# Performance work log

Hardware: AMD Instinct MI355X
Metric: run time of the kernel (lower is better)

The kernel has to match this reference:

```python
import jax, jax.numpy as jnp
import numpy as np

H = 32        # query heads
KV = 8        # kv heads
HD = 128      # head_dim
EPS = 1e-6
THETA = 1e6
T = 2048
D = 4096


def _rms_norm(x, w):
    # x: [T, heads, HD]
    var = jnp.mean(jnp.square(x), axis=-1, keepdims=True)
    return x * jax.lax.rsqrt(var + EPS) * w


def _rope(x, cos, sin):
    # NEOX-style rotary: split last dim in halves. x: [T, heads, HD]
    x1, x2 = jnp.split(x, 2, axis=-1)
    return jnp.concatenate([x1 * cos - x2 * sin, x2 * cos + x1 * sin], axis=-1)


def setup_inputs() -> dict:
    key = jax.random.key(0)
    k1, k2, k3 = jax.random.split(key, 3)
    s = 1.0 / np.sqrt(D)
    return {
        "positions": jnp.arange(T, dtype=jnp.int32),
        "hidden_states": jax.random.normal(k1, (T, D), dtype=jnp.float32),
        "w_qkv": jax.random.normal(k2, (D, (H + 2 * KV) * HD), dtype=jnp.float32) * s,
        "q_norm_w": jnp.ones((HD,), dtype=jnp.float32),
        "k_norm_w": jnp.ones((HD,), dtype=jnp.float32),
        "w_o": jax.random.normal(k3, (H * HD, D), dtype=jnp.float32) * s,
    }


def reference(positions, hidden_states, w_qkv, q_norm_w, k_norm_w, w_o):
    scale = HD ** -0.5
    qkv = hidden_states @ w_qkv                              # [T, (H+2KV)*HD]
    q = qkv[:, : H * HD].reshape(T, H, HD)
    k = qkv[:, H * HD : (H + KV) * HD].reshape(T, KV, HD)
    v = qkv[:, (H + KV) * HD :].reshape(T, KV, HD)

    # per-head RMSNorm on q/k (Qwen3 QK-norm)
    q = _rms_norm(q, q_norm_w)
    k = _rms_norm(k, k_norm_w)

    # RoPE
    inv_freq = 1.0 / (THETA ** (jnp.arange(0, HD, 2, dtype=jnp.float32) / HD))
    freqs = positions.astype(jnp.float32)[:, None] * inv_freq  # [T, HD/2]
    cos = jnp.cos(freqs)[:, None, :]                            # [T, 1, HD/2]
    sin = jnp.sin(freqs)[:, None, :]
    q = _rope(q, cos, sin)
    k = _rope(k, cos, sin)

    # GQA: repeat kv heads
    rep = H // KV
    k = jnp.repeat(k, rep, axis=1)                           # [T, H, HD]
    v = jnp.repeat(v, rep, axis=1)

    # causal SDPA
    scores = jnp.einsum("thd,shd->hts", q, k) * scale        # [H, T, T]
    causal = jnp.tril(jnp.ones((T, T), dtype=bool))
    scores = jnp.where(causal[None], scores, jnp.finfo(scores.dtype).min)
    probs = jax.nn.softmax(scores, axis=-1)
    attn = jnp.einsum("hts,shd->thd", probs, v).reshape(T, H * HD)

    return attn @ w_o                                        # [T, D]
```

## Files before the change

### kernel.cpp

```cpp
#include <hip/hip_runtime.h>

#define TT   2048
#define DD   4096
#define NH   32
#define NKVH 8
#define HDM  128
#define KD   4096
#define NQKV 6144

typedef unsigned short u16;
typedef short v8s __attribute__((ext_vector_type(8)));
typedef float v4f __attribute__((ext_vector_type(4)));

#define QSCALE 0.12751744547734565f
#define EOFF   17.312340490667562f

__device__ __forceinline__ u16 f2bf(float f) {
    unsigned u = __builtin_bit_cast(unsigned, f);
    u += 0x7fffu + ((u >> 16) & 1u);
    return (u16)(u >> 16);
}
__device__ __forceinline__ float bf2f(u16 h) {
    return __builtin_bit_cast(float, ((unsigned)h) << 16);
}
__device__ __forceinline__ void gl2lds16(const void* g, void* l) {
    using gv = const __attribute__((address_space(1))) void;
    using lv = __attribute__((address_space(3))) void;
    __builtin_amdgcn_global_load_lds((gv*)g, (lv*)l, 16, 0, 0);
}

__device__ __forceinline__ void transpose_tile64(const float* __restrict__ in,
                                                 u16* __restrict__ out,
                                                 int K, int N, int n0, int k0,
                                                 float* tile, int t) {
    int rc = t >> 4, cc = (t & 15) * 4;
#pragma unroll
    for (int p = 0; p < 4; ++p) {
        int k = p * 16 + rc;
        float4 v = *(const float4*)&in[(size_t)(k0 + k) * N + n0 + cc];
        tile[k * 65 + cc] = v.x; tile[k * 65 + cc + 1] = v.y;
        tile[k * 65 + cc + 2] = v.z; tile[k * 65 + cc + 3] = v.w;
    }
    __syncthreads();
    int rn = t >> 3, ck = (t & 7) * 8;
#pragma unroll
    for (int p = 0; p < 2; ++p) {
        int n = p * 32 + rn;
        v8s tv;
#pragma unroll
        for (int j = 0; j < 8; ++j) tv[j] = (short)f2bf(tile[(ck + j) * 65 + n]);
        *(v8s*)&out[(size_t)(n0 + n) * K + k0 + ck] = tv;
    }
}

__global__ __launch_bounds__(256) void prep_all_kernel(const float* __restrict__ hidden,
                                                       u16* __restrict__ hid_bf,
                                                       const int* __restrict__ positions,
                                                       float* __restrict__ cosT,
                                                       float* __restrict__ sinT,
                                                       const float* __restrict__ w_qkv,
                                                       u16* __restrict__ wqkv_t) {
    __shared__ float tile[64 * 65];
    int b = blockIdx.x;
    if (b < 4096) {
        size_t i = ((size_t)b * 256 + threadIdx.x) * 8;
        float4 a = *(const float4*)&hidden[i];
        float4 c = *(const float4*)&hidden[i + 4];
        v8s tv;
        tv[0] = (short)f2bf(a.x); tv[1] = (short)f2bf(a.y);
        tv[2] = (short)f2bf(a.z); tv[3] = (short)f2bf(a.w);
        tv[4] = (short)f2bf(c.x); tv[5] = (short)f2bf(c.y);
        tv[6] = (short)f2bf(c.z); tv[7] = (short)f2bf(c.w);
        *(v8s*)&hid_bf[i] = tv;
    } else if (b < 4608) {
        int idx = (b - 4096) * 256 + threadIdx.x;
        int tp = idx >> 6, i = idx & 63;
        float invf = exp2f(-(float)i * 0.31143075889569023f);
        float f = (float)positions[tp] * invf;
        cosT[idx] = cosf(f);
        sinT[idx] = sinf(f);
    } else {
        int bx = b - 4608;
        int n0 = (bx % 96) * 64, k0 = (bx / 96) * 64;
        transpose_tile64(w_qkv, wqkv_t, 4096, NQKV, n0, k0, tile, threadIdx.x);
    }
}

__global__ __launch_bounds__(256) void gemm_bt_kernel(
    const u16* __restrict__ A, const u16* __restrict__ Bt, float* __restrict__ C, int N)
{
    __shared__ __align__(16) u16 smem[16896];
    u16* As = smem;
    u16* Bs = smem + 8192;
    int tid = threadIdx.x;
    int wave = tid >> 6, lane = tid & 63;
    int quad = lane >> 4, l15 = lane & 15;
    int lm = l15 & 7;
    int wm = wave >> 1, wn = wave & 1;
    int m0 = blockIdx.y * 128, n0 = blockIdx.x * 128;

    v4f acc[4][4];
    v4f z4 = {0.f, 0.f, 0.f, 0.f};
#pragma unroll
    for (int mi = 0; mi < 4; ++mi)
#pragma unroll
        for (int ni = 0; ni < 4; ++ni) acc[mi][ni] = z4;

    int rsub = lane >> 3;
    int cg = (lane & 7) ^ rsub;
    const u16* Ag = &A[(size_t)m0 * KD + cg * 8];
    const u16* Bg = &Bt[(size_t)n0 * KD + cg * 8];

    for (int k0 = 0; k0 < KD; k0 += 64) {
        __syncthreads();
#pragma unroll
        for (int c = 0; c < 4; ++c) {
            int ch = wave * 4 + c;
            int row = ch * 8 + rsub;
            gl2lds16(&Ag[(size_t)row * KD + k0], &As[ch * 512]);
            gl2lds16(&Bg[(size_t)row * KD + k0], &Bs[ch * 512]);
        }
        __syncthreads();
#pragma unroll
        for (int ks = 0; ks < 2; ++ks) {
            v8s af[4], bfr[4];
#pragma unroll
            for (int mi = 0; mi < 4; ++mi) {
                int ar = wm * 64 + mi * 16 + l15;
                af[mi] = *(const v8s*)&As[ar * 64 + ((((ks << 2) + quad) ^ lm) << 3)];
            }
#pragma unroll
            for (int ni = 0; ni < 4; ++ni) {
                int br = wn * 64 + ni * 16 + l15;
                bfr[ni] = *(const v8s*)&Bs[br * 64 + ((((ks << 2) + quad) ^ lm) << 3)];
            }
#pragma unroll
            for (int mi = 0; mi < 4; ++mi)
#pragma unroll
                for (int ni = 0; ni < 4; ++ni)
                    acc[mi][ni] = __builtin_amdgcn_mfma_f32_16x16x32_bf16(
                        af[mi], bfr[ni], acc[mi][ni], 0, 0, 0);
        }
    }
#pragma unroll
    for (int mi = 0; mi < 4; ++mi)
#pragma unroll
        for (int ni = 0; ni < 4; ++ni)
#pragma unroll
            for (int r = 0; r < 4; ++r)
                C[(size_t)(m0 + wm * 64 + mi * 16 + quad * 4 + r) * N +
                  (n0 + wn * 64 + ni * 16 + l15)] = acc[mi][ni][r];
}

__global__ __launch_bounds__(512, 2) void gemm_qkv384_kernel(
    const u16* __restrict__ A, const u16* __restrict__ Bt,
    const float* __restrict__ qw, const float* __restrict__ kw,
    const float* __restrict__ cosT, const float* __restrict__ sinT,
    u16* __restrict__ Qb, u16* __restrict__ Kb, u16* __restrict__ Vt)
{
    __shared__ __align__(16) char smem_raw[131072];
    u16* lds = (u16*)smem_raw;
    const int tid = threadIdx.x;
    const int wave = tid >> 6, lane = tid & 63;
    const int quad = lane >> 4, l15 = lane & 15, lm = l15 & 7;
    const int wm = wave >> 2, wn = wave & 3;
    const int m0 = blockIdx.y * 128, n0 = blockIdx.x * 384;

    v4f acc[2][4][3];
    v4f z4 = {0.f, 0.f, 0.f, 0.f};
#pragma unroll
    for (int nh = 0; nh < 2; ++nh)
#pragma unroll
        for (int mi = 0; mi < 4; ++mi)
#pragma unroll
            for (int ni = 0; ni < 3; ++ni) acc[nh][mi][ni] = z4;

    const int rsub = lane >> 3;
    const int cg = (lane & 7) ^ rsub;
    const int ch0 = wave * 2;
    const int g0 = (quad ^ lm) << 3;
    const int g1 = ((4 + quad) ^ lm) << 3;

    const u16* AgR0 = &A[((size_t)m0 + (ch0 + 0) * 8 + rsub) * KD + cg * 8];
    const u16* AgR1 = &A[((size_t)m0 + (ch0 + 1) * 8 + rsub) * KD + cg * 8];
    const u16* BgR0 = &Bt[((size_t)n0 + (ch0 + 0) * 8 + rsub) * KD + cg * 8];
    const u16* BgR1 = &Bt[((size_t)n0 + (ch0 + 1) * 8 + rsub) * KD + cg * 8];

#define STAGE_AH(tt) do { \
    int _b = ((tt) & 1) * 32768; \
    gl2lds16(AgR0 + (size_t)(tt) * 64, &lds[_b + (ch0 + 0) * 512]); \
    gl2lds16(AgR1 + (size_t)(tt) * 64, &lds[_b + (ch0 + 1) * 512]); \
  } while (0)
#define STAGE_BH(tt, h) do { \
    int _b = ((tt) & 1) * 32768 + 8192; \
    gl2lds16(BgR0 + (size_t)(h) * 128 * KD + (size_t)(tt) * 64, \
             &lds[_b + (h) * 8192 + (ch0 + 0) * 512]); \
    gl2lds16(BgR1 + (size_t)(h) * 128 * KD + (size_t)(tt) * 64, \
             &lds[_b + (h) * 8192 + (ch0 + 1) * 512]); \
  } while (0)

    v8s af[4], bfr[3];

#define PHASEX(BO, G, NHI, RDA, STAGE_CODE, WAIT_CODE) do { \
    if (RDA) { \
      _Pragma("unroll") \
      for (int mi = 0; mi < 4; ++mi) \
        af[mi] = *(const v8s*)&lds[(BO) + (wm * 64 + mi * 16 + l15) * 64 + (G)]; \
    } \
    _Pragma("unroll") \
    for (int ni = 0; ni < 3; ++ni) \
      bfr[ni] = *(const v8s*)&lds[(BO) + 8192 + \
                   (wn * 96 + (NHI) * 48 + ni * 16 + l15) * 64 + (G)]; \
    STAGE_CODE; \
    __builtin_amdgcn_s_barrier(); \
    asm volatile("s_waitcnt lgkmcnt(0)" ::: "memory"); \
    __builtin_amdgcn_s_setprio(1); \
    _Pragma("unroll") \
    for (int mi = 0; mi < 4; ++mi) \
      _Pragma("unroll") \
      for (int ni = 0; ni < 3; ++ni) \
        acc[NHI][mi][ni] = __builtin_amdgcn_mfma_f32_16x16x32_bf16( \
            af[mi], bfr[ni], acc[NHI][mi][ni], 0, 0, 0); \
    __builtin_amdgcn_s_setprio(0); \
    WAIT_CODE; \
    __builtin_amdgcn_s_barrier(); \
  } while (0)

#define VM0 asm volatile("s_waitcnt vmcnt(0)" ::: "memory")

#define TILE_MAIN(BO, TT1) do { \
    PHASEX(BO, g0, 0, 1, { STAGE_AH(TT1); STAGE_BH(TT1, 0); }, {}); \
    PHASEX(BO, g0, 1, 0, { STAGE_BH(TT1, 1); }, {}); \
    PHASEX(BO, g1, 0, 1, { STAGE_BH(TT1, 2); }, {}); \
    PHASEX(BO, g1, 1, 0, {}, { VM0; }); \
  } while (0)

    STAGE_AH(0); STAGE_BH(0, 0); STAGE_BH(0, 1); STAGE_BH(0, 2);
    VM0;
    __builtin_amdgcn_s_barrier();

#pragma unroll 2
    for (int t = 0; t < 62; ++t) {
        const int bo = (t & 1) * 32768;
        TILE_MAIN(bo, t + 1);
    }
    TILE_MAIN(0, 63);
    PHASEX(32768, g0, 0, 1, {}, {});
    PHASEX(32768, g0, 1, 0, {}, {});
    PHASEX(32768, g1, 0, 1, {}, {});
    PHASEX(32768, g1, 1, 0, {}, {});
#undef TILE_MAIN
#undef PHASEX
#undef STAGE_AH
#undef STAGE_BH
#undef VM0

    u16* Ct = lds;
    const int t0q = blockIdx.y * 128;
    __syncthreads();
#pragma unroll
    for (int nh = 0; nh < 2; ++nh)
#pragma unroll
        for (int mi = 0; mi < 4; ++mi)
#pragma unroll
            for (int ni = 0; ni < 3; ++ni)
#pragma unroll
                for (int r = 0; r < 4; ++r)
                    Ct[(wm * 64 + mi * 16 + quad * 4 + r) * 392 +
                       wn * 96 + nh * 48 + ni * 16 + l15] = f2bf(acc[nh][mi][ni][r]);
    __syncthreads();
    if (tid < 384) {
        const int row = tid & 127, hh = tid >> 7;
        const int head = blockIdx.x * 3 + hh;
        if (head < 40) {
            const float* w = (head < 32) ? qw : kw;
            float ss = 0.f;
            for (int i = 0; i < 128; ++i) {
                float x = bf2f(Ct[row * 392 + hh * 128 + i]);
                ss += x * x;
            }
            float rs = rsqrtf(ss * (1.0f / 128.0f) + 1e-6f);
            if (head < 32) rs *= QSCALE;
            const int ti = t0q + row;
            for (int i = 0; i < 64; ++i) {
                float x1 = bf2f(Ct[row * 392 + hh * 128 + i]) * rs * w[i];
                float x2 = bf2f(Ct[row * 392 + hh * 128 + 64 + i]) * rs * w[64 + i];
                float c = cosT[ti * 64 + i], s = sinT[ti * 64 + i];
                Ct[row * 392 + hh * 128 + i]      = f2bf(x1 * c - x2 * s);
                Ct[row * 392 + hh * 128 + 64 + i] = f2bf(x2 * c + x1 * s);
            }
        }
    }
    __syncthreads();
#pragma unroll
    for (int hh = 0; hh < 3; ++hh) {
        const int head = blockIdx.x * 3 + hh;
        if (head < 40) {
            u16* dst = (head < 32) ? &Qb[((size_t)head * TT + t0q) * HDM]
                                   : &Kb[((size_t)(head - 32) * TT + t0q) * HDM];
            for (int cix = tid; cix < 128 * 16; cix += 512) {
                int row = cix >> 4, part = (cix & 15) * 8;
                v8s tv;
#pragma unroll
                for (int j = 0; j < 8; ++j) tv[j] = (short)Ct[row * 392 + hh * 128 + part + j];
                *(v8s*)&dst[row * HDM + part] = tv;
            }
        } else {
            const int kvh = head - 40;
            for (int cix = tid; cix < 128 * 16; cix += 512) {
                int hd = cix >> 4, tb = cix & 15;
                v8s tv;
#pragma unroll
                for (int j = 0; j < 8; ++j) tv[j] = (short)Ct[(tb * 8 + j) * 392 + hh * 128 + hd];
                *(v8s*)&Vt[((size_t)kvh * HDM + hd) * TT + t0q + tb * 8] = tv;
            }
        }
    }
}

__global__ __launch_bounds__(256) void attn_plus_kernel(
    const u16* __restrict__ Qb, const u16* __restrict__ Kb,
    const u16* __restrict__ Vt, u16* __restrict__ Ob,
    const float* __restrict__ w_o, u16* __restrict__ wo_t)
{
    __shared__ __align__(16) char smem_raw[40960];
    int tid = threadIdx.x;
    if (blockIdx.x >= 1024) {
        int bx = blockIdx.x - 1024;
        int n0 = (bx & 63) * 64, k0 = (bx >> 6) * 64;
        transpose_tile64(w_o, wo_t, 4096, 4096, n0, k0, (float*)smem_raw, tid);
        return;
    }
    u16* Kl = (u16*)smem_raw;
    u16* Vl = (u16*)(smem_raw + 16384);
    u16* Pl = (u16*)(smem_raw + 32768);
    int wave = tid >> 6, lane = tid & 63;
    int quad = lane >> 4, l15 = lane & 15;
    int idx = blockIdx.x;
    int h = idx & 31;
    int qb = 31 - (idx >> 5);
    int kv = h >> 2;
    int q0 = qb * 64;
    int lm = l15 & 7;

    v8s qf[4];
    {
        const u16* qr = &Qb[((size_t)h * TT + q0 + wave * 16 + l15) * HDM];
#pragma unroll
        for (int ks = 0; ks < 4; ++ks) qf[ks] = *(const v8s*)&qr[ks * 32 + quad * 8];
    }

    v4f z4 = {0.f, 0.f, 0.f, 0.f};
    v4f of[8];
#pragma unroll
    for (int i = 0; i < 8; ++i) of[i] = z4;
    float lsum[4];
#pragma unroll
    for (int r = 0; r < 4; ++r) lsum[r] = 0.f;
    u16* Pw = &Pl[wave * 1024];

    for (int s0 = 0; s0 <= q0; s0 += 64) {
        __syncthreads();
#pragma unroll
        for (int c = 0; c < 4; ++c) {
            int ch = wave * 4 + c;
            int rk = ch * 4 + (lane >> 4);
            int ck = (lane & 15) ^ (rk & 7);
            gl2lds16(&Kb[((size_t)kv * TT + s0 + rk) * HDM + ck * 8], &Kl[ch * 512]);
            int rv = ch * 8 + (lane >> 3);
            int cv = (lane & 7) ^ (rv & 7);
            gl2lds16(&Vt[((size_t)kv * HDM + rv) * TT + s0 + cv * 8], &Vl[ch * 512]);
        }
        __syncthreads();
        v4f sf[4];
#pragma unroll
        for (int nt = 0; nt < 4; ++nt) {
            v4f cacc = z4;
#pragma unroll
            for (int ks = 0; ks < 4; ++ks)
                cacc = __builtin_amdgcn_mfma_f32_16x16x32_bf16(
                    qf[ks],
                    *(const v8s*)&Kl[(nt * 16 + l15) * 128 + (((ks * 4 + quad) ^ lm) << 3)],
                    cacc, 0, 0, 0);
            sf[nt] = cacc;
        }
        if (s0 == q0) {
#pragma unroll
            for (int nt = 0; nt < 4; ++nt) {
                int sg = s0 + nt * 16 + l15;
#pragma unroll
                for (int r = 0; r < 4; ++r) {
                    int qg = q0 + wave * 16 + quad * 4 + r;
                    if (sg > qg) sf[nt][r] = -3.0e38f;
                }
            }
        }
#pragma unroll
        for (int nt = 0; nt < 4; ++nt)
#pragma unroll
            for (int r = 0; r < 4; ++r) {
                float p = exp2f(sf[nt][r] - EOFF);
                sf[nt][r] = p;
                lsum[r] += p;
            }
#pragma unroll
        for (int nt = 0; nt < 4; ++nt)
#pragma unroll
            for (int r = 0; r < 4; ++r) {
                int row = quad * 4 + r;
                int pch = ((nt << 1) + (l15 >> 3)) ^ (row & 7);
                Pw[row * 64 + pch * 8 + (l15 & 7)] = f2bf(sf[nt][r]);
            }
#pragma unroll
        for (int sub = 0; sub < 2; ++sub) {
            v8s pa = *(const v8s*)&Pw[l15 * 64 + ((((sub << 2) + quad) ^ lm) << 3)];
#pragma unroll
            for (int nt = 0; nt < 8; ++nt)
                of[nt] = __builtin_amdgcn_mfma_f32_16x16x32_bf16(
                    pa,
                    *(const v8s*)&Vl[(nt * 16 + l15) * 64 + ((((sub << 2) + quad) ^ lm) << 3)],
                    of[nt], 0, 0, 0);
        }
    }
#pragma unroll
    for (int off = 1; off < 16; off <<= 1)
#pragma unroll
        for (int r = 0; r < 4; ++r) lsum[r] += __shfl_xor(lsum[r], off, 64);
    float invl[4];
#pragma unroll
    for (int r = 0; r < 4; ++r) invl[r] = 1.0f / lsum[r];
#pragma unroll
    for (int nt = 0; nt < 8; ++nt)
#pragma unroll
        for (int r = 0; r < 4; ++r)
            Ob[(size_t)(q0 + wave * 16 + quad * 4 + r) * (NH * HDM) + h * HDM + nt * 16 + l15] =
                f2bf(of[nt][r] * invl[r]);
}

extern "C" void kernel_launch(void* const* d_in, const int* in_sizes, int n_in,
                              void* d_out, int out_size, void* d_ws, size_t ws_size,
                              hipStream_t stream)
{
    (void)in_sizes; (void)n_in; (void)out_size; (void)ws_size;
    const int*   positions = (const int*)d_in[0];
    const float* hidden    = (const float*)d_in[1];
    const float* w_qkv     = (const float*)d_in[2];
    const float* q_norm_w  = (const float*)d_in[3];
    const float* k_norm_w  = (const float*)d_in[4];
    const float* w_o       = (const float*)d_in[5];
    float* out = (float*)d_out;
    char* ws = (char*)d_ws;
    char* ob = (char*)d_out;

    u16* hid_bf = (u16*)(ws + 0);
    u16* attnO  = (u16*)(ws + 0);
    u16* wqkv_t = (u16*)(ws + (size_t)16777216);
    u16* wo_t   = (u16*)(ws + (size_t)16777216);

    u16*   Qb   = (u16*)(ob + 0);
    u16*   Kb   = (u16*)(ob + (size_t)16777216);
    u16*   Vt   = (u16*)(ob + (size_t)20971520);
    float* cosT = (float*)(ob + (size_t)25165824);
    float* sinT = (float*)(ob + (size_t)25690112);

    prep_all_kernel<<<10752, 256, 0, stream>>>(hidden, hid_bf, positions, cosT, sinT,
                                               w_qkv, wqkv_t);

    gemm_qkv384_kernel<<<dim3(16, 16), 512, 0, stream>>>(
        hid_bf, wqkv_t, q_norm_w, k_norm_w, cosT, sinT, Qb, Kb, Vt);

    attn_plus_kernel<<<5120, 256, 0, stream>>>(Qb, Kb, Vt, attnO, w_o, wo_t);

    gemm_bt_kernel<<<dim3(32, 16), 256, 0, stream>>>(attnO, wo_t, out, 4096);
}
```

Before: 456.9 us.

## Pipeline output GEMM with double-buffered LDS and 128x256 tiles

Replaces the simple single-buffered output projection GEMM with a 512-thread, 128x256-tile kernel. It double-buffers global-to-LDS loads so the next K tile is fetched while MFMAs run, and raises wave priority around the MFMAs. The QKV kernel also drops an explicit lgkmcnt wait, changes its LDS row stride from 392 to 390 to reduce bank conflicts, and reorders V-transpose indexing. The tradeoffs are higher LDS and register pressure, and dropping the lgkmcnt wait depends on compiler-inserted waits for correctness.

```diff
diff --git a/kernel.cpp b/kernel.cpp
--- a/kernel.cpp
+++ b/kernel.cpp
@@ -14,6 +14,7 @@
 
 #define QSCALE 0.12751744547734565f
 #define EOFF   17.312340490667562f
+#define CTS 390
 
 __device__ __forceinline__ u16 f2bf(float f) {
     unsigned u = __builtin_bit_cast(unsigned, f);
@@ -86,18 +87,16 @@
     }
 }
 
-__global__ __launch_bounds__(256) void gemm_bt_kernel(
-    const u16* __restrict__ A, const u16* __restrict__ Bt, float* __restrict__ C, int N)
+__global__ __launch_bounds__(512, 2) void gemm_out_kernel(
+    const u16* __restrict__ A, const u16* __restrict__ Bt, float* __restrict__ C)
 {
-    __shared__ __align__(16) u16 smem[16896];
-    u16* As = smem;
-    u16* Bs = smem + 8192;
-    int tid = threadIdx.x;
-    int wave = tid >> 6, lane = tid & 63;
-    int quad = lane >> 4, l15 = lane & 15;
-    int lm = l15 & 7;
-    int wm = wave >> 1, wn = wave & 1;
-    int m0 = blockIdx.y * 128, n0 = blockIdx.x * 128;
+    __shared__ __align__(16) char smem_raw[98304];
+    u16* lds = (u16*)smem_raw;
+    const int tid = threadIdx.x;
+    const int wave = tid >> 6, lane = tid & 63;
+    const int quad = lane >> 4, l15 = lane & 15, lm = l15 & 7;
+    const int wm = wave >> 2, wn = wave & 3;
+    const int m0 = blockIdx.y * 128, n0 = blockIdx.x * 256;
 
     v4f acc[4][4];
     v4f z4 = {0.f, 0.f, 0.f, 0.f};
@@ -106,49 +105,80 @@
 #pragma unroll
         for (int ni = 0; ni < 4; ++ni) acc[mi][ni] = z4;
 
-    int rsub = lane >> 3;
-    int cg = (lane & 7) ^ rsub;
-    const u16* Ag = &A[(size_t)m0 * KD + cg * 8];
-    const u16* Bg = &Bt[(size_t)n0 * KD + cg * 8];
-
-    for (int k0 = 0; k0 < KD; k0 += 64) {
-        __syncthreads();
-#pragma unroll
-        for (int c = 0; c < 4; ++c) {
-            int ch = wave * 4 + c;
-            int row = ch * 8 + rsub;
-            gl2lds16(&Ag[(size_t)row * KD + k0], &As[ch * 512]);
-            gl2lds16(&Bg[(size_t)row * KD + k0], &Bs[ch * 512]);
-        }
-        __syncthreads();
-#pragma unroll
-        for (int ks = 0; ks < 2; ++ks) {
-            v8s af[4], bfr[4];
-#pragma unroll
-            for (int mi = 0; mi < 4; ++mi) {
-                int ar = wm * 64 + mi * 16 + l15;
-                af[mi] = *(const v8s*)&As[ar * 64 + ((((ks << 2) + quad) ^ lm) << 3)];
-            }
-#pragma unroll
-            for (int ni = 0; ni < 4; ++ni) {
-                int br = wn * 64 + ni * 16 + l15;
-                bfr[ni] = *(const v8s*)&Bs[br * 64 + ((((ks << 2) + quad) ^ lm) << 3)];
-            }
-#pragma unroll
-            for (int mi = 0; mi < 4; ++mi)
-#pragma unroll
-                for (int ni = 0; ni < 4; ++ni)
-                    acc[mi][ni] = __builtin_amdgcn_mfma_f32_16x16x32_bf16(
-                        af[mi], bfr[ni], acc[mi][ni], 0, 0, 0);
-        }
-    }
+    const int rsub = lane >> 3;
+    const int cg = (lane & 7) ^ rsub;
+    const int ch0a = wave * 2, ch0b = wave * 4;
+    const int g0 = (quad ^ lm) << 3;
+    const int g1 = ((4 + quad) ^ lm) << 3;
+
+    const u16* AgR0 = &A[((size_t)m0 + (ch0a + 0) * 8 + rsub) * KD + cg * 8];
+    const u16* AgR1 = &A[((size_t)m0 + (ch0a + 1) * 8 + rsub) * KD + cg * 8];
+    const u16* BgR0 = &Bt[((size_t)n0 + (ch0b + 0) * 8 + rsub) * KD + cg * 8];
+    const u16* BgR1 = &Bt[((size_t)n0 + (ch0b + 1) * 8 + rsub) * KD + cg * 8];
+    const u16* BgR2 = &Bt[((size_t)n0 + (ch0b + 2) * 8 + rsub) * KD + cg * 8];
+    const u16* BgR3 = &Bt[((size_t)n0 + (ch0b + 3) * 8 + rsub) * KD + cg * 8];
+
+#define OSTAGE(tt) do { \
+    int _b = ((tt) & 1) * 24576; \
+    gl2lds16(AgR0 + (size_t)(tt) * 64, &lds[_b + (ch0a + 0) * 512]); \
+    gl2lds16(AgR1 + (size_t)(tt) * 64, &lds[_b + (ch0a + 1) * 512]); \
+    gl2lds16(BgR0 + (size_t)(tt) * 64, &lds[_b + 8192 + (ch0b + 0) * 512]); \
+    gl2lds16(BgR1 + (size_t)(tt) * 64, &lds[_b + 8192 + (ch0b + 1) * 512]); \
+    gl2lds16(BgR2 + (size_t)(tt) * 64, &lds[_b + 8192 + (ch0b + 2) * 512]); \
+    gl2lds16(BgR3 + (size_t)(tt) * 64, &lds[_b + 8192 + (ch0b + 3) * 512]); \
+  } while (0)
+
+    v8s af[4], bfr[4];
+
+#define OPHASE(BO, G, STAGE_CODE, WAIT_CODE) do { \
+    _Pragma("unroll") \
+    for (int mi = 0; mi < 4; ++mi) \
+        af[mi] = *(const v8s*)&lds[(BO) + (wm * 64 + mi * 16 + l15) * 64 + (G)]; \
+    _Pragma("unroll") \
+    for (int ni = 0; ni < 4; ++ni) \
+        bfr[ni] = *(const v8s*)&lds[(BO) + 8192 + (wn * 64 + ni * 16 + l15) * 64 + (G)]; \
+    STAGE_CODE; \
+    __builtin_amdgcn_s_barrier(); \
+    asm volatile("" ::: "memory"); \
+    __builtin_amdgcn_s_setprio(1); \
+    _Pragma("unroll") \
+    for (int mi = 0; mi < 4; ++mi) \
+      _Pragma("unroll") \
+      for (int ni = 0; ni < 4; ++ni) \
+        acc[mi][ni] = __builtin_amdgcn_mfma_f32_16x16x32_bf16( \
+            af[mi], bfr[ni], acc[mi][ni], 0, 0, 0); \
+    __builtin_amdgcn_s_setprio(0); \
+    WAIT_CODE; \
+    __builtin_amdgcn_s_barrier(); \
+  } while (0)
+
+#define VM0 asm volatile("s_waitcnt vmcnt(0)" ::: "memory")
+
+    OSTAGE(0);
+    VM0;
+    __builtin_amdgcn_s_barrier();
+
+#pragma unroll 2
+    for (int t = 0; t < 62; ++t) {
+        const int bo = (t & 1) * 24576;
+        OPHASE(bo, g0, { OSTAGE(t + 1); }, {});
+        OPHASE(bo, g1, {}, { VM0; });
+    }
+    OPHASE(0, g0, { OSTAGE(63); }, {});
+    OPHASE(0, g1, {}, { VM0; });
+    OPHASE(24576, g0, {}, {});
+    OPHASE(24576, g1, {}, {});
+#undef OPHASE
+#undef OSTAGE
+#undef VM0
+
 #pragma unroll
     for (int mi = 0; mi < 4; ++mi)
 #pragma unroll
         for (int ni = 0; ni < 4; ++ni)
 #pragma unroll
             for (int r = 0; r < 4; ++r)
-                C[(size_t)(m0 + wm * 64 + mi * 16 + quad * 4 + r) * N +
+                C[(size_t)(m0 + wm * 64 + mi * 16 + quad * 4 + r) * 4096 +
                   (n0 + wn * 64 + ni * 16 + l15)] = acc[mi][ni][r];
 }
 
@@ -213,7 +243,7 @@
                    (wn * 96 + (NHI) * 48 + ni * 16 + l15) * 64 + (G)]; \
     STAGE_CODE; \
     __builtin_amdgcn_s_barrier(); \
-    asm volatile("s_waitcnt lgkmcnt(0)" ::: "memory"); \
+    asm volatile("" ::: "memory"); \
     __builtin_amdgcn_s_setprio(1); \
     _Pragma("unroll") \
     for (int mi = 0; mi < 4; ++mi) \
@@ -266,7 +296,7 @@
             for (int ni = 0; ni < 3; ++ni)
 #pragma unroll
                 for (int r = 0; r < 4; ++r)
-                    Ct[(wm * 64 + mi * 16 + quad * 4 + r) * 392 +
+                    Ct[(wm * 64 + mi * 16 + quad * 4 + r) * CTS +
                        wn * 96 + nh * 48 + ni * 16 + l15] = f2bf(acc[nh][mi][ni][r]);
     __syncthreads();
     if (tid < 384) {
@@ -276,18 +306,18 @@
             const float* w = (head < 32) ? qw : kw;
             float ss = 0.f;
             for (int i = 0; i < 128; ++i) {
-                float x = bf2f(Ct[row * 392 + hh * 128 + i]);
+                float x = bf2f(Ct[row * CTS + hh * 128 + i]);
                 ss += x * x;
             }
             float rs = rsqrtf(ss * (1.0f / 128.0f) + 1e-6f);
             if (head < 32) rs *= QSCALE;
             const int ti = t0q + row;
             for (int i = 0; i < 64; ++i) {
-                float x1 = bf2f(Ct[row * 392 + hh * 128 + i]) * rs * w[i];
-                float x2 = bf2f(Ct[row * 392 + hh * 128 + 64 + i]) * rs * w[64 + i];
+                float x1 = bf2f(Ct[row * CTS + hh * 128 + i]) * rs * w[i];
+                float x2 = bf2f(Ct[row * CTS + hh * 128 + 64 + i]) * rs * w[64 + i];
                 float c = cosT[ti * 64 + i], s = sinT[ti * 64 + i];
-                Ct[row * 392 + hh * 128 + i]      = f2bf(x1 * c - x2 * s);
-                Ct[row * 392 + hh * 128 + 64 + i] = f2bf(x2 * c + x1 * s);
+                Ct[row * CTS + hh * 128 + i]      = f2bf(x1 * c - x2 * s);
+                Ct[row * CTS + hh * 128 + 64 + i] = f2bf(x2 * c + x1 * s);
             }
         }
     }
@@ -302,16 +332,16 @@
                 int row = cix >> 4, part = (cix & 15) * 8;
                 v8s tv;
 #pragma unroll
-                for (int j = 0; j < 8; ++j) tv[j] = (short)Ct[row * 392 + hh * 128 + part + j];
+                for (int j = 0; j < 8; ++j) tv[j] = (short)Ct[row * CTS + hh * 128 + part + j];
                 *(v8s*)&dst[row * HDM + part] = tv;
             }
         } else {
             const int kvh = head - 40;
             for (int cix = tid; cix < 128 * 16; cix += 512) {
-                int hd = cix >> 4, tb = cix & 15;
+                int hd = cix & 127, tb = cix >> 7;
                 v8s tv;
 #pragma unroll
-                for (int j = 0; j < 8; ++j) tv[j] = (short)Ct[(tb * 8 + j) * 392 + hh * 128 + hd];
+                for (int j = 0; j < 8; ++j) tv[j] = (short)Ct[(tb * 8 + j) * CTS + hh * 128 + hd];
                 *(v8s*)&Vt[((size_t)kvh * HDM + hd) * TT + t0q + tb * 8] = tv;
             }
         }
@@ -471,5 +501,5 @@
 
     attn_plus_kernel<<<5120, 256, 0, stream>>>(Qb, Kb, Vt, attnO, w_o, wo_t);
 
-    gemm_bt_kernel<<<dim3(32, 16), 256, 0, stream>>>(attnO, wo_t, out, 4096);
-}
+    gemm_out_kernel<<<dim3(16, 16), 512, 0, stream>>>(attnO, wo_t, out);
+}
```

Result: no change. 451.3 us (-1.2%).
